# Kernel tuning notes

Measured on AMD Instinct MI355X. Metric: run time of the kernel, lower is better.

The kernel has to match this reference:

```python
import jax, jax.numpy as jnp
import numpy as np

N_QUBITS = 14
N_LAYERS = 6
BATCH = 512
DIM = 2 ** N_QUBITS

# Z expectation sign table: qubit 0 is the most-significant bit of the state index
_idx = np.arange(DIM)
_bits = np.stack([(_idx >> (N_QUBITS - 1 - q)) & 1 for q in range(N_QUBITS)])  # [n, DIM]
SIGNS = jnp.asarray(1.0 - 2.0 * _bits, dtype=jnp.float32)  # +1 for bit 0, -1 for bit 1


def _rx(theta):
    # 2x2 RX(theta) = [[cos(t/2), -i sin(t/2)], [-i sin(t/2), cos(t/2)]]
    c = jnp.cos(theta / 2).astype(jnp.complex64)
    s = ((-1j) * jnp.sin(theta / 2)).astype(jnp.complex64)
    return jnp.stack([jnp.stack([c, s]), jnp.stack([s, c])])


def _apply_1q(state, mat, q):
    # state: [B, 2^n] complex; apply 2x2 mat on qubit q
    left = 2 ** q
    right = 2 ** (N_QUBITS - 1 - q)
    s = state.reshape(-1, left, 2, right)
    s = jnp.einsum('ij,bljr->blir', mat, s)
    return s.reshape(-1, DIM)


def _apply_cnot(state, c, t):
    # CNOT(control=c, target=t): flip target bit where control bit is 1
    hi, lo = (c, t) if c < t else (t, c)
    A = 2 ** hi
    M = 2 ** (lo - hi - 1)
    R = 2 ** (N_QUBITS - 1 - lo)
    s = state.reshape(-1, A, 2, M, 2, R)
    if c < t:
        flipped = jnp.flip(s[:, :, 1:2, :, :, :], axis=4)
        s = jnp.concatenate([s[:, :, 0:1, :, :, :], flipped], axis=2)
    else:
        flipped = jnp.flip(s[:, :, :, :, 1:2, :], axis=2)
        s = jnp.concatenate([s[:, :, :, :, 0:1, :], flipped], axis=4)
    return s.reshape(-1, DIM)


def _forward(x, params):
    B = x.shape[0]
    # angle embedding in X basis: product state of RX(x_q)|0> per qubit
    half = 0.5 * x
    amps = jnp.stack([jnp.cos(half).astype(jnp.complex64),
                      ((-1j) * jnp.sin(half)).astype(jnp.complex64)], axis=-1)  # [B, n, 2]
    state = amps[:, 0]
    for q in range(1, N_QUBITS):
        state = (state[:, :, None] * amps[:, q][:, None, :]).reshape(B, -1)
    # basic_entangling ansatz: per-qubit RX then ring of CNOTs, per layer
    for layer in range(N_LAYERS):
        w = params[layer, 0]  # [n_qubits]
        for q in range(N_QUBITS):
            state = _apply_1q(state, _rx(w[q]), q)
        for q in range(N_QUBITS):
            state = _apply_cnot(state, q, (q + 1) % N_QUBITS)
    # <Z_q> expectation per qubit
    probs = state.real ** 2 + state.imag ** 2  # [B, DIM]
    return probs @ SIGNS.T  # [B, n_qubits]


def setup_inputs():
    key = jax.random.key(0)
    k1, k2 = jax.random.split(key)
    x = jax.random.normal(k1, (BATCH, N_QUBITS), dtype=jnp.float32)
    params = 2.0 * jnp.pi * jax.random.uniform(k2, (N_LAYERS, 1, N_QUBITS), dtype=jnp.float32)
    return {"x": x, "params": params}


def reference(x, params):
    return _forward(x, params)
```

## Files before the change

kernel.cpp:

```cpp
#include <hip/hip_runtime.h>
#include <math.h>


#define NQ 14
#define DIM 16384
#define NLAYERS 6
#define NGATES (NLAYERS * NQ)
#define BATCH 512
#define T2 256
#define TB 1024
#define NREP 16

constexpr int cpopc(unsigned v) { int c = 0; while (v) { c += (int)(v & 1u); v >>= 1; } return c; }

constexpr unsigned cpext(unsigned v, unsigned m) {
    unsigned r = 0; int b = 0;
    for (int pos = 0; pos < 16; ++pos)
        if ((m >> pos) & 1u) { r |= ((v >> pos) & 1u) << b; ++b; }
    return r;
}

struct Tabs {
    unsigned short m[NGATES];
    unsigned short r[NQ];
    int p[NQ];
    int off[NQ + 1];
    unsigned char qb[NQ][NQ];
    int ng[NQ];
    unsigned short gmask[NQ][NGATES];
    unsigned char  gidx[NQ][NGATES];
};

constexpr Tabs gen_tabs() {
    Tabs T{};
    unsigned short C[NQ] = {}, R[NQ] = {};
    for (int q = 0; q < NQ; ++q) { C[q] = (unsigned short)(1u << (NQ - 1 - q)); R[q] = C[q]; }
    for (int l = 0; l < NLAYERS; ++l) {
        for (int q = 0; q < NQ; ++q) T.m[l * NQ + q] = C[q];
        for (int g = 0; g < NQ; ++g) {
            int t = (g + 1) % NQ;
            C[g] ^= C[t];
            R[t] ^= R[g];
        }
    }
    for (int q = 0; q < NQ; ++q) T.r[q] = R[q];
    for (int q = 0; q < NQ; ++q) {
        int cnt = 0;
        for (int pos = 0; pos < NQ; ++pos)
            if ((R[q] >> pos) & 1u) { T.qb[q][cnt] = (unsigned char)(NQ - 1 - pos); ++cnt; }
        T.p[q] = cnt;
    }
    T.off[0] = 0;
    for (int q = 0; q < NQ; ++q) T.off[q + 1] = T.off[q] + (1 << T.p[q]);
    for (int q = 0; q < NQ; ++q) {
        int n = 0;
        for (int g = 0; g < NGATES; ++g) {
            if (cpopc((unsigned)(T.m[g] & R[q])) & 1) {
                T.gmask[q][n] = T.m[g];
                T.gidx[q][n]  = (unsigned char)g;
                ++n;
            }
        }
        T.ng[q] = n;
    }
    return T;
}
constexpr Tabs TAB = gen_tabs();

constexpr int calc_maxp() { int m = 0; for (int q = 0; q < NQ; ++q) if (TAB.p[q] > m) m = TAB.p[q]; return m; }
constexpr int calc_minp() { int m = 99; for (int q = 0; q < NQ; ++q) if (TAB.p[q] < m) m = TAB.p[q]; return m; }
constexpr int MAXP  = calc_maxp();
constexpr int MINP  = calc_minp();
constexpr int TOTAL = TAB.off[NQ];
static_assert(MAXP <= 8, "u = t & (2^p-1) needs p <= 10; replicas sized for p <= 8");
static_assert(MINP >= 1, "r mask must be nonzero");

template<int Q, int I>
__device__ __forceinline__ void gates(const float2* __restrict__ w, int t,
                                      float (&Bx)[16], float (&By)[16])
{
    if constexpr (I < TAB.ng[Q]) {
        constexpr unsigned r  = TAB.r[Q];
        constexpr unsigned nr = (~r) & 0x3FFFu;
        constexpr int      p  = TAB.p[Q];
        constexpr unsigned mg = TAB.gmask[Q][I];
        constexpr unsigned Ag = cpext(mg, r);
        constexpr unsigned Bg = cpext(mg, nr);
        constexpr unsigned Mg = Ag | ((Bg & ((1u << (10 - p)) - 1u)) << p);
        constexpr unsigned Hg = (Bg >> (10 - p)) & 15u;
        const float2 wv = w[I];
        const float si = (__popc((unsigned)t & Mg) & 1) ? -wv.y : wv.y;
        const float c  = wv.x;
        const float nx = Bx[Hg] * c - By[Hg] * si;
        const float ny = Bx[Hg] * si + By[Hg] * c;
        Bx[Hg] = nx; By[Hg] = ny;
        gates<Q, I + 1>(w, t, Bx, By);
    }
}

template<int Q>
__device__ __forceinline__ void build_q(const float2* __restrict__ w,
                                        float* __restrict__ binC,
                                        float* __restrict__ binS, int t)
{
    constexpr int      p       = TAB.p[Q];
    constexpr unsigned lowmask = (1u << p) - 1u;

    float Bx[16], By[16];
    #pragma unroll
    for (int h = 0; h < 16; ++h) { Bx[h] = 1.0f; By[h] = 0.0f; }
    gates<Q, 0>(w, t, Bx, By);

    #pragma unroll
    for (int s = 1; s < 16; s <<= 1) {
        #pragma unroll
        for (int h = 0; h < 16; ++h) {
            if (!(h & s)) {
                const int h1 = h | s;
                const float p1 = Bx[h] * Bx[h1], p2 = By[h] * By[h1];
                const float p3 = Bx[h] * By[h1], p4 = By[h] * Bx[h1];
                Bx[h]  = p1 - p2;  By[h]  = p3 + p4;
                Bx[h1] = p1 + p2;  By[h1] = p4 - p3;
            }
        }
    }

    float fx = 0.0f, fy = 0.0f;
    #pragma unroll
    for (int h = 0; h < 16; ++h) { fx += Bx[h]; fy += By[h]; }

    const unsigned u   = (unsigned)t & lowmask;
    const int      rep = t >> 6;
    float* bc = binC + (rep << MAXP);
    float* bs = binS + (rep << MAXP);

    if constexpr (p >= 6) {
        bc[u] = fx;
        bs[u] = fy;
    } else {
        constexpr unsigned dm = 63u & ~lowmask;
        #pragma unroll
        for (int bb = p; bb < 6; ++bb) {
            fx += __shfl_xor(fx, 1 << bb, 64);
            fy += __shfl_xor(fy, 1 << bb, 64);
        }
        if (((unsigned)t & dm) == 0u) {
            bc[u] = fx;
            bs[u] = fy;
        }
    }
}

__global__ __launch_bounds__(TB, 4)
void build_tables(const float* __restrict__ params, float* __restrict__ tab)
{
    __shared__ float2 w[NGATES];
    __shared__ float  binC[NREP << MAXP];
    __shared__ float  binS[NREP << MAXP];

    const int q = blockIdx.x;
    const int t = threadIdx.x;
    const int ng = TAB.ng[q];

    if (t < ng) {
        const float th = params[(int)TAB.gidx[q][t]];
        float s, c; sincosf(th, &s, &c);
        w[t] = make_float2(c, s);
    }
    for (int i = t; i < (NREP << MAXP); i += TB) { binC[i] = 0.0f; binS[i] = 0.0f; }
    __syncthreads();

    switch (q) {
        case 0:  build_q<0 >(w, binC, binS, t); break;
        case 1:  build_q<1 >(w, binC, binS, t); break;
        case 2:  build_q<2 >(w, binC, binS, t); break;
        case 3:  build_q<3 >(w, binC, binS, t); break;
        case 4:  build_q<4 >(w, binC, binS, t); break;
        case 5:  build_q<5 >(w, binC, binS, t); break;
        case 6:  build_q<6 >(w, binC, binS, t); break;
        case 7:  build_q<7 >(w, binC, binS, t); break;
        case 8:  build_q<8 >(w, binC, binS, t); break;
        case 9:  build_q<9 >(w, binC, binS, t); break;
        case 10: build_q<10>(w, binC, binS, t); break;
        case 11: build_q<11>(w, binC, binS, t); break;
        case 12: build_q<12>(w, binC, binS, t); break;
        case 13: build_q<13>(w, binC, binS, t); break;
    }
    __syncthreads();

    const int nbins = 1 << TAB.p[q];
    const int off   = TAB.off[q];
    for (int i = t; i < nbins; i += TB) {
        float sc = 0.0f, ss = 0.0f;
        #pragma unroll
        for (int rp = 0; rp < NREP; ++rp) {
            sc += binC[(rp << MAXP) + i];
            ss += binS[(rp << MAXP) + i];
        }
        tab[off + i]         = sc;
        tab[TOTAL + off + i] = ss;
    }
}

__global__ __launch_bounds__(T2)
void qout_kernel(const float* __restrict__ x, const float* __restrict__ tab,
                 float* __restrict__ out)
{
    __shared__ float sx[NQ];
    __shared__ float red[T2 / 64][NQ];

    const int b = blockIdx.x;
    const int t = threadIdx.x;
    if (t < NQ) sx[t] = x[b * NQ + t];
    __syncthreads();

    float acc[NQ];
    #pragma unroll
    for (int q = 0; q < NQ; ++q) acc[q] = 0.0f;

    #pragma unroll
    for (int q = 0; q < NQ; ++q) {
        const int nb  = 1 << TAB.p[q];
        const int off = TAB.off[q];
        for (int u = t; u < nb; u += T2) {
            float A = 0.0f;
            #pragma unroll
            for (int i = 0; i < TAB.p[q]; ++i) {
                const float xv = sx[TAB.qb[q][i]];
                A += ((u >> i) & 1) ? xv : -xv;
            }
            float s, c;
            sincosf(A, &s, &c);
            acc[q] += c * tab[off + u] + s * tab[TOTAL + off + u];
        }
    }

    #pragma unroll
    for (int q = 0; q < NQ; ++q) {
        #pragma unroll
        for (int o = 32; o > 0; o >>= 1)
            acc[q] += __shfl_down(acc[q], o, 64);
    }
    const int wave = t >> 6;
    const int lane = t & 63;
    if (lane == 0) {
        #pragma unroll
        for (int q = 0; q < NQ; ++q) red[wave][q] = acc[q];
    }
    __syncthreads();
    if (t < NQ) {
        float sum = 0.0f;
        #pragma unroll
        for (int w = 0; w < T2 / 64; ++w) sum += red[w][t];
        out[b * NQ + t] = sum * (1.0f / (float)DIM);
    }
}

extern "C" void kernel_launch(void* const* d_in, const int* in_sizes, int n_in,
                              void* d_out, int out_size, void* d_ws, size_t ws_size,
                              hipStream_t stream) {
    const float* x      = (const float*)d_in[0];
    const float* params = (const float*)d_in[1];
    float* out          = (float*)d_out;
    float* tab          = (float*)d_ws;

    build_tables<<<NQ, TB, 0, stream>>>(params, tab);
    qout_kernel<<<BATCH, T2, 0, stream>>>(x, tab, out);
}
```

Before: 68.34 us.

## Fuse table build and per-sample evaluation into one kernel over qubit-slice blocks

```diff
diff --git a/kernel.cpp b/kernel.cpp
--- a/kernel.cpp
+++ b/kernel.cpp
@@ -7,9 +7,11 @@
 #define NLAYERS 6
 #define NGATES (NLAYERS * NQ)
 #define BATCH 512
-#define T2 256
 #define TB 1024
 #define NREP 16
+#define NSLICE 16
+#define SLICE_B (BATCH / NSLICE)
+#define B_PER_WAVE (SLICE_B * 64 / TB)
 
 constexpr int cpopc(unsigned v) { int c = 0; while (v) { c += (int)(v & 1u); v >>= 1; } return c; }
 
@@ -151,16 +153,73 @@
     }
 }
 
+template<int Q>
+__device__ __forceinline__ void run_q(const float2* __restrict__ w,
+                                      float* __restrict__ binC,
+                                      float* __restrict__ binS,
+                                      float* __restrict__ tabC,
+                                      float* __restrict__ tabS,
+                                      const float* __restrict__ sxAll,
+                                      float* __restrict__ out,
+                                      int slice, int t)
+{
+    build_q<Q>(w, binC, binS, t);
+    __syncthreads();
+
+    constexpr int p  = TAB.p[Q];
+    constexpr int nb = 1 << p;
+    for (int i = t; i < nb; i += TB) {
+        float sc = 0.0f, ss = 0.0f;
+        #pragma unroll
+        for (int rp = 0; rp < NREP; ++rp) {
+            sc += binC[(rp << MAXP) + i];
+            ss += binS[(rp << MAXP) + i];
+        }
+        tabC[i] = sc;
+        tabS[i] = ss;
+    }
+    __syncthreads();
+
+    const int wave = t >> 6;
+    const int lane = t & 63;
+    #pragma unroll
+    for (int bb = 0; bb < B_PER_WAVE; ++bb) {
+        const int bl = wave * B_PER_WAVE + bb;
+        float acc = 0.0f;
+        for (int u = lane; u < nb; u += 64) {
+            float A = 0.0f;
+            #pragma unroll
+            for (int i = 0; i < p; ++i) {
+                const float xv = sxAll[bl * NQ + TAB.qb[Q][i]];
+                A += ((u >> i) & 1) ? xv : -xv;
+            }
+            float s, c;
+            sincosf(A, &s, &c);
+            acc += c * tabC[u] + s * tabS[u];
+        }
+        #pragma unroll
+        for (int o = 32; o > 0; o >>= 1)
+            acc += __shfl_down(acc, o, 64);
+        if (lane == 0)
+            out[(slice * SLICE_B + bl) * NQ + Q] = acc * (1.0f / (float)DIM);
+    }
+}
+
 __global__ __launch_bounds__(TB, 4)
-void build_tables(const float* __restrict__ params, float* __restrict__ tab)
+void fused_kernel(const float* __restrict__ x, const float* __restrict__ params,
+                  float* __restrict__ out)
 {
     __shared__ float2 w[NGATES];
     __shared__ float  binC[NREP << MAXP];
     __shared__ float  binS[NREP << MAXP];
-
-    const int q = blockIdx.x;
-    const int t = threadIdx.x;
-    const int ng = TAB.ng[q];
+    __shared__ float  tabC[1 << MAXP];
+    __shared__ float  tabS[1 << MAXP];
+    __shared__ float  sxAll[SLICE_B * NQ];
+
+    const int q     = blockIdx.x % NQ;
+    const int slice = blockIdx.x / NQ;
+    const int t     = threadIdx.x;
+    const int ng    = TAB.ng[q];
 
     if (t < ng) {
         const float th = params[(int)TAB.gidx[q][t]];
@@ -168,91 +227,24 @@
         w[t] = make_float2(c, s);
     }
     for (int i = t; i < (NREP << MAXP); i += TB) { binC[i] = 0.0f; binS[i] = 0.0f; }
+    for (int i = t; i < SLICE_B * NQ; i += TB)   sxAll[i] = x[slice * (SLICE_B * NQ) + i];
     __syncthreads();
 
     switch (q) {
-        case 0:  build_q<0 >(w, binC, binS, t); break;
-        case 1:  build_q<1 >(w, binC, binS, t); break;
-        case 2:  build_q<2 >(w, binC, binS, t); break;
-        case 3:  build_q<3 >(w, binC, binS, t); break;
-        case 4:  build_q<4 >(w, binC, binS, t); break;
-        case 5:  build_q<5 >(w, binC, binS, t); break;
-        case 6:  build_q<6 >(w, binC, binS, t); break;
-        case 7:  build_q<7 >(w, binC, binS, t); break;
-        case 8:  build_q<8 >(w, binC, binS, t); break;
-        case 9:  build_q<9 >(w, binC, binS, t); break;
-        case 10: build_q<10>(w, binC, binS, t); break;
-        case 11: build_q<11>(w, binC, binS, t); break;
-        case 12: build_q<12>(w, binC, binS, t); break;
-        case 13: build_q<13>(w, binC, binS, t); break;
-    }
-    __syncthreads();
-
-    const int nbins = 1 << TAB.p[q];
-    const int off   = TAB.off[q];
-    for (int i = t; i < nbins; i += TB) {
-        float sc = 0.0f, ss = 0.0f;
-        #pragma unroll
-        for (int rp = 0; rp < NREP; ++rp) {
-            sc += binC[(rp << MAXP) + i];
-            ss += binS[(rp << MAXP) + i];
-        }
-        tab[off + i]         = sc;
-        tab[TOTAL + off + i] = ss;
-    }
-}
-
-__global__ __launch_bounds__(T2)
-void qout_kernel(const float* __restrict__ x, const float* __restrict__ tab,
-                 float* __restrict__ out)
-{
-    __shared__ float sx[NQ];
-    __shared__ float red[T2 / 64][NQ];
-
-    const int b = blockIdx.x;
-    const int t = threadIdx.x;
-    if (t < NQ) sx[t] = x[b * NQ + t];
-    __syncthreads();
-
-    float acc[NQ];
-    #pragma unroll
-    for (int q = 0; q < NQ; ++q) acc[q] = 0.0f;
-
-    #pragma unroll
-    for (int q = 0; q < NQ; ++q) {
-        const int nb  = 1 << TAB.p[q];
-        const int off = TAB.off[q];
-        for (int u = t; u < nb; u += T2) {
-            float A = 0.0f;
-            #pragma unroll
-            for (int i = 0; i < TAB.p[q]; ++i) {
-                const float xv = sx[TAB.qb[q][i]];
-                A += ((u >> i) & 1) ? xv : -xv;
-            }
-            float s, c;
-            sincosf(A, &s, &c);
-            acc[q] += c * tab[off + u] + s * tab[TOTAL + off + u];
-        }
-    }
-
-    #pragma unroll
-    for (int q = 0; q < NQ; ++q) {
-        #pragma unroll
-        for (int o = 32; o > 0; o >>= 1)
-            acc[q] += __shfl_down(acc[q], o, 64);
-    }
-    const int wave = t >> 6;
-    const int lane = t & 63;
-    if (lane == 0) {
-        #pragma unroll
-        for (int q = 0; q < NQ; ++q) red[wave][q] = acc[q];
-    }
-    __syncthreads();
-    if (t < NQ) {
-        float sum = 0.0f;
-        #pragma unroll
-        for (int w = 0; w < T2 / 64; ++w) sum += red[w][t];
-        out[b * NQ + t] = sum * (1.0f / (float)DIM);
+        case 0:  run_q<0 >(w, binC, binS, tabC, tabS, sxAll, out, slice, t); break;
+        case 1:  run_q<1 >(w, binC, binS, tabC, tabS, sxAll, out, slice, t); break;
+        case 2:  run_q<2 >(w, binC, binS, tabC, tabS, sxAll, out, slice, t); break;
+        case 3:  run_q<3 >(w, binC, binS, tabC, tabS, sxAll, out, slice, t); break;
+        case 4:  run_q<4 >(w, binC, binS, tabC, tabS, sxAll, out, slice, t); break;
+        case 5:  run_q<5 >(w, binC, binS, tabC, tabS, sxAll, out, slice, t); break;
+        case 6:  run_q<6 >(w, binC, binS, tabC, tabS, sxAll, out, slice, t); break;
+        case 7:  run_q<7 >(w, binC, binS, tabC, tabS, sxAll, out, slice, t); break;
+        case 8:  run_q<8 >(w, binC, binS, tabC, tabS, sxAll, out, slice, t); break;
+        case 9:  run_q<9 >(w, binC, binS, tabC, tabS, sxAll, out, slice, t); break;
+        case 10: run_q<10>(w, binC, binS, tabC, tabS, sxAll, out, slice, t); break;
+        case 11: run_q<11>(w, binC, binS, tabC, tabS, sxAll, out, slice, t); break;
+        case 12: run_q<12>(w, binC, binS, tabC, tabS, sxAll, out, slice, t); break;
+        case 13: run_q<13>(w, binC, binS, tabC, tabS, sxAll, out, slice, t); break;
     }
 }
 
@@ -262,8 +254,7 @@
     const float* x      = (const float*)d_in[0];
     const float* params = (const float*)d_in[1];
     float* out          = (float*)d_out;
-    float* tab          = (float*)d_ws;
-
-    build_tables<<<NQ, TB, 0, stream>>>(params, tab);
-    qout_kernel<<<BATCH, T2, 0, stream>>>(x, tab, out);
-}
+    (void)d_ws; (void)ws_size;
+
+    fused_kernel<<<NQ * NSLICE, TB, 0, stream>>>(x, params, out);
+}
```

Measured after the change: 64.29 us. -5.9%, faster.
